# Kernel optimization log

Measured on AMD Instinct MI355X. Metric: run time of the kernel, lower is better.

Reference implementation:

```python
import jax, jax.numpy as jnp
import numpy as np

NUM_HEADS = 3
DIM = 96
MLP_HIDDEN = int(DIM * 4.0)
LN_EPS = 1e-5


def _layernorm(x, g, b):
    mu = jnp.mean(x, axis=-1, keepdims=True)
    var = jnp.mean(jnp.square(x - mu), axis=-1, keepdims=True)
    return (x - mu) * jax.lax.rsqrt(var + LN_EPS) * g + b


def setup_inputs() -> dict:
    key = jax.random.key(0)
    ks = jax.random.split(key, 12)
    B, H, W, T, C = 1, 48, 48, 48, DIM
    L = H * W * T
    s = 0.02
    return {
        "x": jax.random.normal(ks[0], (B, L, C), dtype=jnp.float32),
        "mask_matrix": jnp.zeros((1, 1), dtype=jnp.float32),
        "ln1_g": jnp.ones((C,), jnp.float32),
        "ln1_b": jnp.zeros((C,), jnp.float32),
        "qkv_w": jax.random.normal(ks[1], (3 * C, C), jnp.float32) * s,
        "qkv_b": jnp.zeros((3 * C,), jnp.float32),
        "proj_w": jax.random.normal(ks[2], (C, C), jnp.float32) * s,
        "proj_b": jnp.zeros((C,), jnp.float32),
        "ln2_g": jnp.ones((C,), jnp.float32),
        "ln2_b": jnp.zeros((C,), jnp.float32),
        "fc1_w": jax.random.normal(ks[3], (MLP_HIDDEN, C), jnp.float32) * s,
        "fc1_b": jnp.zeros((MLP_HIDDEN,), jnp.float32),
        "fc2_w": jax.random.normal(ks[4], (C, MLP_HIDDEN), jnp.float32) * s,
        "fc2_b": jnp.zeros((C,), jnp.float32),
        "H": 48, "W": 48, "T": 48,
    }


def reference(x, mask_matrix, ln1_g, ln1_b, qkv_w, qkv_b, proj_w, proj_b,
              ln2_g, ln2_b, fc1_w, fc1_b, fc2_w, fc2_b, H, W, T):
    B, L, C = x.shape
    nh = NUM_HEADS
    hd = C // nh
    scale = hd ** -0.5

    shortcut = x
    h = _layernorm(x, ln1_g, ln1_b)
    # [B,H,W,T,C] -> permute(0,3,1,2,4) -> [B*T, H*W, C]  (axial_dims='12', extra_dim=3)
    h = h.reshape(B, H, W, T, C).transpose(0, 3, 1, 2, 4).reshape(B * T, H * W, C)
    B_, N, _ = h.shape

    qkv = h @ qkv_w.T + qkv_b                       # [B_, N, 3C]
    # faithful to torch: permute(1,0,2) -> reshape(1,N,3,nh,B_*hd) -> permute(2,0,3,1,4)
    qkv = jnp.transpose(qkv, (1, 0, 2)).reshape(1, N, 3, nh, B_ * hd)
    qkv = jnp.transpose(qkv, (2, 0, 3, 1, 4))       # [3, 1, nh, N, B_*hd]
    q, k, v = qkv[0] * scale, qkv[1], qkv[2]

    attn = jax.nn.softmax(q @ jnp.swapaxes(k, -2, -1), axis=-1)  # [1, nh, N, N]
    o = attn @ v                                    # [1, nh, N, B_*hd]
    o = jnp.transpose(o, (0, 2, 1, 3)).reshape(B_, N, C)
    o = o @ proj_w.T + proj_b
    # faithful to torch: plain view back to [B, H*W*T, C] (no inverse permute)
    o = o.reshape(B, H * W * T, C)

    x = shortcut + o
    h2 = _layernorm(x, ln2_g, ln2_b)
    m = jax.nn.gelu(h2 @ fc1_w.T + fc1_b, approximate=False) @ fc2_w.T + fc2_b
    return x + m
```

## Files before the change

### kernel.cpp

```cpp
#include <hip/hip_runtime.h>
#include <hip/hip_bf16.h>
#include <math.h>

typedef __bf16 bf16_t;
typedef __bf16 bf16x8 __attribute__((ext_vector_type(8)));
typedef __bf16 bf16x4 __attribute__((ext_vector_type(4)));
typedef float f32x4 __attribute__((ext_vector_type(4)));

#define AS1q __attribute__((address_space(1)))
#define AS3q __attribute__((address_space(3)))

__device__ __forceinline__ void gload_lds16(const bf16_t* g, bf16_t* l) {
    __builtin_amdgcn_global_load_lds((AS1q void*)g, (AS3q void*)l, 16, 0, 0);
}

#define LROWS   110592
#define CDIM    96
#define NTOK    2304
#define FDIM    1536
#define YSTR    3538944ll
#define SSTR    5308416ll
#define SCALE_Q 0.1767766952966369f

__global__ __launch_bounds__(256)
void conv_w(const float* __restrict__ a, const float* __restrict__ b,
            const float* __restrict__ c, const float* __restrict__ d,
            bf16_t* __restrict__ out)
{
    int i = blockIdx.x * 256 + threadIdx.x;
    float v;
    if (i < 27648)       v = a[i];
    else if (i < 36864)  v = b[i - 27648];
    else if (i < 73728)  v = c[i - 36864];
    else                 v = d[i - 73728];
    out[i] = (bf16_t)v;
}

__global__ __launch_bounds__(256)
void ln4_kernel(const float* __restrict__ x, const float* __restrict__ gamma,
                const float* __restrict__ beta, bf16_t* __restrict__ out, int permute)
{
    int wave = threadIdx.x >> 6;
    int half = (threadIdx.x >> 5) & 1;
    int cl   = threadIdx.x & 31;
    int row  = blockIdx.x * 8 + wave * 2 + half;
    bool act = cl < 24;
    const f32x4* xr = (const f32x4*)(x + (size_t)row * CDIM);
    f32x4 v = {0.f, 0.f, 0.f, 0.f};
    if (act) v = xr[cl];
    float s = v[0] + v[1] + v[2] + v[3];
    #pragma unroll
    for (int off = 16; off > 0; off >>= 1) s += __shfl_xor(s, off, 64);
    float mean = s * (1.f / 96.f);
    f32x4 d = {0.f, 0.f, 0.f, 0.f};
    if (act) { d[0]=v[0]-mean; d[1]=v[1]-mean; d[2]=v[2]-mean; d[3]=v[3]-mean; }
    float vs = d[0]*d[0] + d[1]*d[1] + d[2]*d[2] + d[3]*d[3];
    #pragma unroll
    for (int off = 16; off > 0; off >>= 1) vs += __shfl_xor(vs, off, 64);
    float rstd = rsqrtf(vs * (1.f / 96.f) + 1e-5f);
    size_t orow = row;
    if (permute) { int t = row % 48; int n = row / 48; orow = (size_t)t * NTOK + n; }
    if (act) {
        f32x4 g = ((const f32x4*)gamma)[cl];
        f32x4 b = ((const f32x4*)beta)[cl];
        bf16x4 o;
        #pragma unroll
        for (int j = 0; j < 4; j++) o[j] = (bf16_t)(d[j] * rstd * g[j] + b[j]);
        *(bf16x4*)(out + orow * CDIM + cl * 4) = o;
    }
}

__global__ __launch_bounds__(256)
void softmax_k(const bf16_t* __restrict__ S, bf16_t* __restrict__ P,
               long long sZ, long long pZ)
{
    int wv = threadIdx.x >> 6, lane = threadIdx.x & 63;
    int row = blockIdx.x * 4 + wv;
    const bf16_t* sr = S + (size_t)blockIdx.z * sZ + (size_t)row * NTOK;
    bf16_t* pr = P + (size_t)blockIdx.z * pZ + (size_t)row * NTOK;
    float v[36];
    float mx = -1e30f;
    #pragma unroll
    for (int t = 0; t < 9; t++) {
        bf16x4 c = *(const bf16x4*)(sr + (size_t)(t * 64 + lane) * 4);
        #pragma unroll
        for (int j = 0; j < 4; j++) { v[t*4+j] = (float)c[j]; mx = fmaxf(mx, v[t*4+j]); }
    }
    #pragma unroll
    for (int off = 32; off > 0; off >>= 1) mx = fmaxf(mx, __shfl_xor(mx, off, 64));
    float sum = 0.f;
    #pragma unroll
    for (int j = 0; j < 36; j++) { v[j] = __expf(v[j] - mx); sum += v[j]; }
    #pragma unroll
    for (int off = 32; off > 0; off >>= 1) sum += __shfl_xor(sum, off, 64);
    float inv = 1.f / sum;
    #pragma unroll
    for (int t = 0; t < 9; t++) {
        bf16x4 o;
        #pragma unroll
        for (int j = 0; j < 4; j++) o[j] = (bf16_t)(v[t*4+j] * inv);
        *(bf16x4*)(pr + (size_t)(t * 64 + lane) * 4) = o;
    }
}

template<int BN, int EPI, int NBY>
__global__ __launch_bounds__(256, 2)
void gemm_bt(const bf16_t* __restrict__ A, const bf16_t* __restrict__ W,
             void* __restrict__ out, int K,
             long long aZ, long long wZ, long long oZ, float scale)
{
    constexpr int BM = 128, BK = 64;
    constexpr int MI = 4;
    constexpr int NT = BN / 32;
    constexpr int NB = 18 * NBY;
    constexpr int CHK = (NB + 7) / 8;
    __shared__ bf16_t As[BM * BK];
    __shared__ bf16_t Bs[BN * BK];

    int id = blockIdx.x;
    int id2 = (id & 7) * CHK + (id >> 3);
    if (id2 >= NB) return;
    int p  = id2 / 108;
    int r_ = id2 - p * 108;
    int by = p * 6 + (r_ % 6);
    int bx = r_ / 6;

    const int tid = threadIdx.x;
    const int wave = tid >> 6, lane = tid & 63;
    const int quad = lane >> 4, l16 = lane & 15;
    const int wm = wave & 1, wn = wave >> 1;
    const int z = blockIdx.z;
    A += (size_t)z * aZ;
    W += (size_t)z * wZ;
    const int m0 = bx * BM, n0 = by * BN;

    f32x4 acc[MI][NT];
    #pragma unroll
    for (int i = 0; i < MI; i++)
        #pragma unroll
        for (int j = 0; j < NT; j++) { f32x4 zz = {0.f, 0.f, 0.f, 0.f}; acc[i][j] = zz; }

    const int srow = lane >> 3;
    const int scol = lane & 7;

    for (int k0 = 0; k0 < K; k0 += BK) {
        __syncthreads();
        for (int it = wave; it < BM / 8; it += 4) {
            int r = it * 8 + srow;
            int cg = scol ^ (r & 7);
            gload_lds16(A + (size_t)(m0 + r) * K + k0 + cg * 8, &As[it * 512]);
        }
        for (int it = wave; it < BN / 8; it += 4) {
            int r = it * 8 + srow;
            int cg = scol ^ (r & 7);
            gload_lds16(W + (size_t)(n0 + r) * K + k0 + cg * 8, &Bs[it * 512]);
        }
        __syncthreads();

        bf16x8 af[MI][2], bfr[NT][2];
        #pragma unroll
        for (int i = 0; i < MI; i++) {
            int r = wm * 64 + i * 16 + l16;
            #pragma unroll
            for (int kk = 0; kk < 2; kk++)
                af[i][kk] = *(const bf16x8*)&As[r * 64 + (((kk * 4 + quad) ^ (r & 7)) << 3)];
        }
        #pragma unroll
        for (int j = 0; j < NT; j++) {
            int c = wn * (BN / 2) + j * 16 + l16;
            #pragma unroll
            for (int kk = 0; kk < 2; kk++)
                bfr[j][kk] = *(const bf16x8*)&Bs[c * 64 + (((kk * 4 + quad) ^ (c & 7)) << 3)];
        }
        #pragma unroll
        for (int kk = 0; kk < 2; kk++)
            #pragma unroll
            for (int i = 0; i < MI; i++)
                #pragma unroll
                for (int j = 0; j < NT; j++)
                    acc[i][j] = __builtin_amdgcn_mfma_f32_16x16x32_bf16(af[i][kk], bfr[j][kk], acc[i][j], 0, 0, 0);
    }

    #pragma unroll
    for (int i = 0; i < MI; i++)
        #pragma unroll
        for (int j = 0; j < NT; j++)
            #pragma unroll
            for (int ri = 0; ri < 4; ri++) {
                int r = m0 + wm * 64 + i * 16 + quad * 4 + ri;
                int c = n0 + wn * (BN / 2) + j * 16 + l16;
                float v = acc[i][j][ri];
                if constexpr (EPI == 1) {
                    bf16_t* op = (bf16_t*)out + (size_t)z * oZ;
                    op[(size_t)r * NTOK + c] = (bf16_t)(v * scale);
                } else {
                    int b = r / 48, rr = r - b * 48;
                    ((bf16_t*)out)[((size_t)(b * NTOK + rr * 48 + z * 16)) * CDIM + c] = (bf16_t)v;
                }
            }
}

template<int N, int K, int KC, int EPI>
__global__ __launch_bounds__(256, 2)
void gemm_ws(const bf16_t* __restrict__ A, const bf16_t* __restrict__ Wg,
             void* __restrict__ out, const float* __restrict__ bias,
             const float* __restrict__ resid,
             bf16_t* __restrict__ out2, const float* __restrict__ g2,
             const float* __restrict__ b2)
{
    constexpr int KP = K + 8;
    constexpr int NT = N / 16;
    constexpr int KI = KC / 32;
    __shared__ __attribute__((aligned(16))) bf16_t Ws[N * KP];

    const int tid = threadIdx.x;
    const int wave = tid >> 6, lane = tid & 63;
    const int quad = lane >> 4, l16 = lane & 15;
    const int m0 = blockIdx.x * 256;

    constexpr int CH = N * K / 8;
    for (int c = tid; c < CH; c += 256) {
        int row = c / (K / 8), kc = c - row * (K / 8);
        bf16x8 w = *(const bf16x8*)(Wg + row * K + kc * 8);
        *(bf16x8*)(Ws + row * KP + kc * 8) = w;
    }
    __syncthreads();

    const bf16_t* Ar = A + (size_t)(m0 + wave * 64 + l16) * K + quad * 8;

    const int t = m0 / NTOK;
    const int nb = m0 - t * NTOK;

    auto epi_tile = [&](int nt, const f32x4* a4) {
        int c = nt * 16 + l16;
        if constexpr (EPI == 0) {
            int jj = t * 288 + c;
            int g = jj / FDIM, mm = jj - g * FDIM;
            float bv = bias[c];
            if (g < 6) {
                bf16_t* yp = (bf16_t*)out + (size_t)g * YSTR + mm;
                #pragma unroll
                for (int i = 0; i < 4; i++)
                    #pragma unroll
                    for (int ri = 0; ri < 4; ri++) {
                        int n = nb + wave * 64 + i * 16 + quad * 4 + ri;
                        yp[(size_t)n * FDIM] = (bf16_t)(a4[i][ri] + bv);
                    }
            } else {
                bf16_t* vp = out2 + (size_t)(g - 6) * YSTR + (size_t)mm * NTOK;
                #pragma unroll
                for (int i = 0; i < 4; i++) {
                    int n0q = nb + wave * 64 + i * 16 + quad * 4;
                    bf16x4 o;
                    #pragma unroll
                    for (int ri = 0; ri < 4; ri++) o[ri] = (bf16_t)(a4[i][ri] + bv);
                    *(bf16x4*)(vp + n0q) = o;
                }
            }
        } else {
            float bv = bias[c];
            #pragma unroll
            for (int i = 0; i < 4; i++)
                #pragma unroll
                for (int ri = 0; ri < 4; ri++) {
                    int r = m0 + wave * 64 + i * 16 + quad * 4 + ri;
                    float v = a4[i][ri] + bv;
                    if constexpr (EPI == 3) {
                        v = 0.5f * v * (1.0f + erff(v * 0.70710678118654752f));
                        ((bf16_t*)out)[(size_t)r * N + c] = (bf16_t)v;
                    } else {
                        ((float*)out)[(size_t)r * N + c] = v + resid[(size_t)r * N + c];
                    }
                }
        }
    };

    if constexpr (KC == K && EPI != 5) {
        bf16x8 af[4][KI];
        #pragma unroll
        for (int i = 0; i < 4; i++)
            #pragma unroll
            for (int kk = 0; kk < KI; kk++)
                af[i][kk] = *(const bf16x8*)(Ar + (size_t)i * 16 * K + kk * 32);
        #pragma unroll 2
        for (int nt = 0; nt < NT; nt++) {
            bf16x8 bfr[KI];
            #pragma unroll
            for (int kk = 0; kk < KI; kk++)
                bfr[kk] = *(const bf16x8*)(Ws + (nt * 16 + l16) * KP + kk * 32 + quad * 8);
            f32x4 a4[4];
            #pragma unroll
            for (int i = 0; i < 4; i++) { f32x4 zz = {0.f, 0.f, 0.f, 0.f}; a4[i] = zz; }
            #pragma unroll
            for (int kk = 0; kk < KI; kk++)
                #pragma unroll
                for (int i = 0; i < 4; i++)
                    a4[i] = __builtin_amdgcn_mfma_f32_16x16x32_bf16(af[i][kk], bfr[kk], a4[i], 0, 0, 0);
            epi_tile(nt, a4);
        }
    } else {
        f32x4 acc[4][NT];
        #pragma unroll
        for (int i = 0; i < 4; i++)
            #pragma unroll
            for (int j = 0; j < NT; j++) { f32x4 zz = {0.f, 0.f, 0.f, 0.f}; acc[i][j] = zz; }
        for (int kc0 = 0; kc0 < K; kc0 += KC) {
            bf16x8 af[4][KI];
            #pragma unroll
            for (int i = 0; i < 4; i++)
                #pragma unroll
                for (int kk = 0; kk < KI; kk++)
                    af[i][kk] = *(const bf16x8*)(Ar + (size_t)i * 16 * K + kc0 + kk * 32);
            #pragma unroll
            for (int nt = 0; nt < NT; nt++) {
                #pragma unroll
                for (int kk = 0; kk < KI; kk++) {
                    bf16x8 b = *(const bf16x8*)(Ws + (nt * 16 + l16) * KP + kc0 + kk * 32 + quad * 8);
                    #pragma unroll
                    for (int i = 0; i < 4; i++)
                        acc[i][nt] = __builtin_amdgcn_mfma_f32_16x16x32_bf16(af[i][kk], b, acc[i][nt], 0, 0, 0);
                }
            }
        }
        if constexpr (EPI == 5) {
            float bv[NT], gv[NT], bb[NT];
            #pragma unroll
            for (int nt = 0; nt < NT; nt++) {
                int c = nt * 16 + l16;
                bv[nt] = bias[c]; gv[nt] = g2[c]; bb[nt] = b2[c];
            }
            #pragma unroll
            for (int i = 0; i < 4; i++)
                #pragma unroll
                for (int ri = 0; ri < 4; ri++) {
                    int r = m0 + wave * 64 + i * 16 + quad * 4 + ri;
                    float u[NT];
                    float s = 0.f;
                    #pragma unroll
                    for (int nt = 0; nt < NT; nt++) {
                        int c = nt * 16 + l16;
                        u[nt] = acc[i][nt][ri] + bv[nt] + resid[(size_t)r * N + c];
                        ((float*)out)[(size_t)r * N + c] = u[nt];
                        s += u[nt];
                    }
                    #pragma unroll
                    for (int off = 8; off > 0; off >>= 1) s += __shfl_xor(s, off, 64);
                    float mean = s * (1.f / 96.f);
                    float vs = 0.f;
                    #pragma unroll
                    for (int nt = 0; nt < NT; nt++) {
                        float dd = u[nt] - mean;
                        u[nt] = dd;
                        vs += dd * dd;
                    }
                    #pragma unroll
                    for (int off = 8; off > 0; off >>= 1) vs += __shfl_xor(vs, off, 64);
                    float rstd = rsqrtf(vs * (1.f / 96.f) + 1e-5f);
                    #pragma unroll
                    for (int nt = 0; nt < NT; nt++) {
                        int c = nt * 16 + l16;
                        out2[(size_t)r * N + c] = (bf16_t)(u[nt] * rstd * gv[nt] + bb[nt]);
                    }
                }
        } else {
            #pragma unroll
            for (int nt = 0; nt < NT; nt++) {
                f32x4 a4[4];
                #pragma unroll
                for (int i = 0; i < 4; i++) a4[i] = acc[i][nt];
                epi_tile(nt, a4);
            }
        }
    }
}

__global__ __launch_bounds__(256, 1)
void mlp_fused(const bf16_t* __restrict__ A, const bf16_t* __restrict__ W1g,
               const bf16_t* __restrict__ W2g, const float* __restrict__ b1,
               const float* __restrict__ b2, const float* __restrict__ resid,
               float* __restrict__ out)
{
    constexpr int KP1 = 104;
    __shared__ __attribute__((aligned(16))) bf16_t W1s[384 * KP1];
    __shared__ __attribute__((aligned(16))) bf16_t W2c[96 * 40];
    __shared__ __attribute__((aligned(16))) bf16_t Tb[256 * 40];

    const int tid = threadIdx.x;
    const int wave = tid >> 6, lane = tid & 63;
    const int quad = lane >> 4, l16 = lane & 15;
    const int m0 = blockIdx.x * 256;

    for (int c = tid; c < 384 * 12; c += 256) {
        int row = c / 12, kc = c - row * 12;
        bf16x8 w = *(const bf16x8*)(W1g + row * 96 + kc * 8);
        *(bf16x8*)(W1s + row * KP1 + kc * 8) = w;
    }

    const bf16_t* Ar = A + (size_t)(m0 + wave * 64 + l16) * 96 + quad * 8;
    bf16x8 af[4][3];
    #pragma unroll
    for (int i = 0; i < 4; i++)
        #pragma unroll
        for (int kk = 0; kk < 3; kk++)
            af[i][kk] = *(const bf16x8*)(Ar + (size_t)i * 16 * 96 + kk * 32);

    __syncthreads();

    f32x4 acc2[4][6];
    #pragma unroll
    for (int i = 0; i < 4; i++)
        #pragma unroll
        for (int j = 0; j < 6; j++) { f32x4 zz = {0.f, 0.f, 0.f, 0.f}; acc2[i][j] = zz; }

    for (int c = 0; c < 12; c++) {
        bf16x4 w2r[3];
        #pragma unroll
        for (int q = 0; q < 3; q++) {
            int e = q * 256 + tid;
            int row = e >> 3, sub = e & 7;
            w2r[q] = *(const bf16x4*)(W2g + row * 384 + c * 32 + sub * 4);
        }
        f32x4 a1[4][2];
        #pragma unroll
        for (int i = 0; i < 4; i++)
            #pragma unroll
            for (int s = 0; s < 2; s++) { f32x4 zz = {0.f, 0.f, 0.f, 0.f}; a1[i][s] = zz; }
        #pragma unroll
        for (int s = 0; s < 2; s++) {
            int n = c * 32 + s * 16 + l16;
            #pragma unroll
            for (int kk = 0; kk < 3; kk++) {
                bf16x8 b = *(const bf16x8*)(W1s + n * KP1 + kk * 32 + quad * 8);
                #pragma unroll
                for (int i = 0; i < 4; i++)
                    a1[i][s] = __builtin_amdgcn_mfma_f32_16x16x32_bf16(af[i][kk], b, a1[i][s], 0, 0, 0);
            }
        }
        __syncthreads();
        #pragma unroll
        for (int s = 0; s < 2; s++) {
            int n = c * 32 + s * 16 + l16;
            float bv = b1[n];
            #pragma unroll
            for (int i = 0; i < 4; i++)
                #pragma unroll
                for (int ri = 0; ri < 4; ri++) {
                    float u = a1[i][s][ri] + bv;
                    u = 0.5f * u * (1.0f + erff(u * 0.70710678118654752f));
                    Tb[(wave * 64 + i * 16 + quad * 4 + ri) * 40 + s * 16 + l16] = (bf16_t)u;
                }
        }
        #pragma unroll
        for (int q = 0; q < 3; q++) {
            int e = q * 256 + tid;
            int row = e >> 3, sub = e & 7;
            *(bf16x4*)(W2c + row * 40 + sub * 4) = w2r[q];
        }
        __syncthreads();
        bf16x8 a2[4];
        #pragma unroll
        for (int i = 0; i < 4; i++)
            a2[i] = *(const bf16x8*)(Tb + (wave * 64 + i * 16 + l16) * 40 + quad * 8);
        #pragma unroll
        for (int nt = 0; nt < 6; nt++) {
            bf16x8 b = *(const bf16x8*)(W2c + (nt * 16 + l16) * 40 + quad * 8);
            #pragma unroll
            for (int i = 0; i < 4; i++)
                acc2[i][nt] = __builtin_amdgcn_mfma_f32_16x16x32_bf16(a2[i], b, acc2[i][nt], 0, 0, 0);
        }
    }

    #pragma unroll
    for (int i = 0; i < 4; i++)
        #pragma unroll
        for (int nt = 0; nt < 6; nt++)
            #pragma unroll
            for (int ri = 0; ri < 4; ri++) {
                int r = m0 + wave * 64 + i * 16 + quad * 4 + ri;
                int cc = nt * 16 + l16;
                out[(size_t)r * 96 + cc] = acc2[i][nt][ri] + b2[cc] + resid[(size_t)r * 96 + cc];
            }
}

extern "C" void kernel_launch(void* const* d_in, const int* in_sizes, int n_in,
                              void* d_out, int out_size, void* d_ws, size_t ws_size,
                              hipStream_t stream)
{
    const float* x      = (const float*)d_in[0];
    const float* ln1_g  = (const float*)d_in[2];
    const float* ln1_b  = (const float*)d_in[3];
    const float* qkv_w  = (const float*)d_in[4];
    const float* qkv_b  = (const float*)d_in[5];
    const float* proj_w = (const float*)d_in[6];
    const float* proj_b = (const float*)d_in[7];
    const float* ln2_g  = (const float*)d_in[8];
    const float* ln2_b  = (const float*)d_in[9];
    const float* fc1_w  = (const float*)d_in[10];
    const float* fc1_b  = (const float*)d_in[11];
    const float* fc2_w  = (const float*)d_in[12];
    const float* fc2_b  = (const float*)d_in[13];

    const size_t SZ_WB = 110592ull * 2;
    const size_t SZ_HP = 10616832ull * 2;
    const size_t SZ_Y  = 31850496ull * 2;
    const size_t SZ_YV = 10616832ull * 2;

    char* ws = (char*)d_ws;
    size_t oWB = 0;
    size_t oHP = oWB + SZ_WB;
    size_t oY  = oHP + SZ_HP;
    size_t oYV = oY + SZ_Y;
    size_t oS  = oYV + SZ_YV;

    bf16_t* Wb    = (bf16_t*)(ws + oWB);
    bf16_t* Wqkv  = Wb;
    bf16_t* Wproj = Wb + 27648;
    bf16_t* Wfc1  = Wb + 36864;
    bf16_t* Wfc2  = Wb + 73728;
    bf16_t* hp    = (bf16_t*)(ws + oHP);
    bf16_t* Y     = (bf16_t*)(ws + oY);
    bf16_t* Yv    = (bf16_t*)(ws + oYV);
    bf16_t* Pb    = (bf16_t*)(ws + oY);
    bf16_t* Sb    = (bf16_t*)(ws + oS);
    float*  x2    = (float*)(ws + oS);
    float*  outp  = (float*)d_out;

    dim3 blk(256);

    conv_w<<<dim3(432), blk, 0, stream>>>(qkv_w, proj_w, fc1_w, fc2_w, Wb);
    ln4_kernel<<<dim3(13824), blk, 0, stream>>>(x, ln1_g, ln1_b, hp, 1);
    gemm_ws<288, 96, 96, 0><<<dim3(432), blk, 0, stream>>>(hp, Wqkv, Y, qkv_b,
                                                           nullptr, Yv, nullptr, nullptr);
    gemm_bt<128, 1, 18><<<dim3(328, 1, 3), blk, 0, stream>>>(Y, Y + 3 * YSTR, Sb,
                                                             1536, YSTR, YSTR, SSTR, SCALE_Q);
    softmax_k<<<dim3(576, 1, 3), blk, 0, stream>>>(Sb, Pb, SSTR, SSTR);
    gemm_bt<128, 2, 12><<<dim3(216, 1, 3), blk, 0, stream>>>(Pb, Yv, hp,
                                                             2304, SSTR, YSTR, 0, 0.f);
    gemm_ws<96, 96, 96, 5><<<dim3(432), blk, 0, stream>>>(hp, Wproj, x2, proj_b, x,
                                                          hp, ln2_g, ln2_b);
    mlp_fused<<<dim3(432), blk, 0, stream>>>(hp, Wfc1, Wfc2, fc1_b, fc2_b, x2, outp);
}
```

Measured before the change: 393.2 us.

## Stream fc1 weights per chunk with double buffering and halve MLP row tile

The fused MLP kernel no longer stages the whole fc1 weight matrix in LDS. It streams 32-row chunks of fc1 and fc2 weights into double-buffered LDS, prefetching the next chunk into registers during compute. Rows per block drop from 256 to 128, the grid grows to 864 blocks, and launch bounds ask for 3 blocks per CU, so LDS and register use shrink enough for more blocks to run at once and latency can hide. The cost is more global weight traffic per output row and more barriers per row.

After: 350.3 us. 1.12x faster.

```diff
diff --git a/kernel.cpp b/kernel.cpp
--- a/kernel.cpp
+++ b/kernel.cpp
@@ -374,65 +374,78 @@
     }
 }
 
-__global__ __launch_bounds__(256, 1)
+__global__ __launch_bounds__(256, 3)
 void mlp_fused(const bf16_t* __restrict__ A, const bf16_t* __restrict__ W1g,
                const bf16_t* __restrict__ W2g, const float* __restrict__ b1,
                const float* __restrict__ b2, const float* __restrict__ resid,
                float* __restrict__ out)
 {
     constexpr int KP1 = 104;
-    __shared__ __attribute__((aligned(16))) bf16_t W1s[384 * KP1];
-    __shared__ __attribute__((aligned(16))) bf16_t W2c[96 * 40];
-    __shared__ __attribute__((aligned(16))) bf16_t Tb[256 * 40];
+    __shared__ __attribute__((aligned(16))) bf16_t W1c[2][32 * KP1];
+    __shared__ __attribute__((aligned(16))) bf16_t W2c[2][96 * 40];
+    __shared__ __attribute__((aligned(16))) bf16_t Tb[128 * 40];
 
     const int tid = threadIdx.x;
     const int wave = tid >> 6, lane = tid & 63;
     const int quad = lane >> 4, l16 = lane & 15;
-    const int m0 = blockIdx.x * 256;
-
-    for (int c = tid; c < 384 * 12; c += 256) {
-        int row = c / 12, kc = c - row * 12;
-        bf16x8 w = *(const bf16x8*)(W1g + row * 96 + kc * 8);
-        *(bf16x8*)(W1s + row * KP1 + kc * 8) = w;
-    }
-
-    const bf16_t* Ar = A + (size_t)(m0 + wave * 64 + l16) * 96 + quad * 8;
-    bf16x8 af[4][3];
-    #pragma unroll
-    for (int i = 0; i < 4; i++)
+    const int m0 = blockIdx.x * 128;
+
+    const bf16_t* Ar = A + (size_t)(m0 + wave * 32 + l16) * 96 + quad * 8;
+    bf16x8 af[2][3];
+    #pragma unroll
+    for (int i = 0; i < 2; i++)
         #pragma unroll
         for (int kk = 0; kk < 3; kk++)
             af[i][kk] = *(const bf16x8*)(Ar + (size_t)i * 16 * 96 + kk * 32);
 
+    bf16x4 w1n[3], w2n[3];
+    #pragma unroll
+    for (int q = 0; q < 3; q++) {
+        int e = q * 256 + tid;
+        w1n[q] = *(const bf16x4*)(W1g + e * 4);
+        int row = e >> 3, sub = e & 7;
+        w2n[q] = *(const bf16x4*)(W2g + row * 384 + sub * 4);
+    }
+    #pragma unroll
+    for (int q = 0; q < 3; q++) {
+        int e = q * 256 + tid;
+        int r1 = e / 24, s1 = e - r1 * 24;
+        *(bf16x4*)(&W1c[0][r1 * KP1 + s1 * 4]) = w1n[q];
+        int row = e >> 3, sub = e & 7;
+        *(bf16x4*)(&W2c[0][row * 40 + sub * 4]) = w2n[q];
+    }
     __syncthreads();
 
-    f32x4 acc2[4][6];
-    #pragma unroll
-    for (int i = 0; i < 4; i++)
+    f32x4 acc2[2][6];
+    #pragma unroll
+    for (int i = 0; i < 2; i++)
         #pragma unroll
         for (int j = 0; j < 6; j++) { f32x4 zz = {0.f, 0.f, 0.f, 0.f}; acc2[i][j] = zz; }
 
     for (int c = 0; c < 12; c++) {
-        bf16x4 w2r[3];
-        #pragma unroll
-        for (int q = 0; q < 3; q++) {
-            int e = q * 256 + tid;
-            int row = e >> 3, sub = e & 7;
-            w2r[q] = *(const bf16x4*)(W2g + row * 384 + c * 32 + sub * 4);
-        }
-        f32x4 a1[4][2];
-        #pragma unroll
-        for (int i = 0; i < 4; i++)
+        const int pb = c & 1;
+        if (c < 11) {
+            #pragma unroll
+            for (int q = 0; q < 3; q++) {
+                int e = q * 256 + tid;
+                w1n[q] = *(const bf16x4*)(W1g + (c + 1) * 3072 + e * 4);
+                int row = e >> 3, sub = e & 7;
+                w2n[q] = *(const bf16x4*)(W2g + row * 384 + (c + 1) * 32 + sub * 4);
+            }
+        }
+        f32x4 a1[2][2];
+        #pragma unroll
+        for (int i = 0; i < 2; i++)
             #pragma unroll
             for (int s = 0; s < 2; s++) { f32x4 zz = {0.f, 0.f, 0.f, 0.f}; a1[i][s] = zz; }
         #pragma unroll
         for (int s = 0; s < 2; s++) {
-            int n = c * 32 + s * 16 + l16;
+            int n = s * 16 + l16;
             #pragma unroll
             for (int kk = 0; kk < 3; kk++) {
-                bf16x8 b = *(const bf16x8*)(W1s + n * KP1 + kk * 32 + quad * 8);
-                #pragma unroll
-                for (int i = 0; i < 4; i++)
+                bf16x8 b = *(const bf16x8*)(&W1c[pb][n * KP1 + kk * 32 + quad * 8]);
+                #pragma unroll
+                for (int i = 0; i < 2; i++)
                     a1[i][s] = __builtin_amdgcn_mfma_f32_16x16x32_bf16(af[i][kk], b, a1[i][s], 0, 0, 0);
             }
         }
@@ -442,41 +455,45 @@
             int n = c * 32 + s * 16 + l16;
             float bv = b1[n];
             #pragma unroll
-            for (int i = 0; i < 4; i++)
+            for (int i = 0; i < 2; i++)
                 #pragma unroll
                 for (int ri = 0; ri < 4; ri++) {
                     float u = a1[i][s][ri] + bv;
                     u = 0.5f * u * (1.0f + erff(u * 0.70710678118654752f));
-                    Tb[(wave * 64 + i * 16 + quad * 4 + ri) * 40 + s * 16 + l16] = (bf16_t)u;
+                    Tb[(wave * 32 + i * 16 + quad * 4 + ri) * 40 + s * 16 + l16] = (bf16_t)u;
                 }
         }
-        #pragma unroll
-        for (int q = 0; q < 3; q++) {
-            int e = q * 256 + tid;
-            int row = e >> 3, sub = e & 7;
-            *(bf16x4*)(W2c + row * 40 + sub * 4) = w2r[q];
+        if (c < 11) {
+            #pragma unroll
+            for (int q = 0; q < 3; q++) {
+                int e = q * 256 + tid;
+                int r1 = e / 24, s1 = e - r1 * 24;
+                *(bf16x4*)(&W1c[pb ^ 1][r1 * KP1 + s1 * 4]) = w1n[q];
+                int row = e >> 3, sub = e & 7;
+                *(bf16x4*)(&W2c[pb ^ 1][row * 40 + sub * 4]) = w2n[q];
+            }
         }
         __syncthreads();
-        bf16x8 a2[4];
-        #pragma unroll
-        for (int i = 0; i < 4; i++)
-            a2[i] = *(const bf16x8*)(Tb + (wave * 64 + i * 16 + l16) * 40 + quad * 8);
+        bf16x8 a2[2];
+        #pragma unroll
+        for (int i = 0; i < 2; i++)
+            a2[i] = *(const bf16x8*)(Tb + (wave * 32 + i * 16 + l16) * 40 + quad * 8);
         #pragma unroll
         for (int nt = 0; nt < 6; nt++) {
-            bf16x8 b = *(const bf16x8*)(W2c + (nt * 16 + l16) * 40 + quad * 8);
-            #pragma unroll
-            for (int i = 0; i < 4; i++)
+            bf16x8 b = *(const bf16x8*)(&W2c[pb][(nt * 16 + l16) * 40 + quad * 8]);
+            #pragma unroll
+            for (int i = 0; i < 2; i++)
                 acc2[i][nt] = __builtin_amdgcn_mfma_f32_16x16x32_bf16(a2[i], b, acc2[i][nt], 0, 0, 0);
         }
     }
 
     #pragma unroll
-    for (int i = 0; i < 4; i++)
+    for (int i = 0; i < 2; i++)
         #pragma unroll
         for (int nt = 0; nt < 6; nt++)
             #pragma unroll
             for (int ri = 0; ri < 4; ri++) {
-                int r = m0 + wave * 64 + i * 16 + quad * 4 + ri;
+                int r = m0 + wave * 32 + i * 16 + quad * 4 + ri;
                 int cc = nt * 16 + l16;
                 out[(size_t)r * 96 + cc] = acc2[i][nt][ri] + b2[cc] + resid[(size_t)r * 96 + cc];
             }
@@ -538,5 +555,5 @@
                                                              2304, SSTR, YSTR, 0, 0.f);
     gemm_ws<96, 96, 96, 5><<<dim3(432), blk, 0, stream>>>(hp, Wproj, x2, proj_b, x,
                                                           hp, ln2_g, ln2_b);
-    mlp_fused<<<dim3(432), blk, 0, stream>>>(hp, Wfc1, Wfc2, fc1_b, fc2_b, x2, outp);
-}
+    mlp_fused<<<dim3(864), blk, 0, stream>>>(hp, Wfc1, Wfc2, fc1_b, fc2_b, x2, outp);
+}
```
